# Kernel optimization log

Hardware: AMD Instinct MI355X
Metric: run time of the kernel (lower is better)

Reference implementation:

```python
import jax, jax.numpy as jnp
import numpy as np

V, D, H, L, F, S, HI, DI, TOPK = 50257, 1024, 16, 8, 4096, 1024, 4, 64, 512
DH = D // H
EPS = 1e-6


def rmsnorm(x, w):
    # matches torch: norm = ||x||_2 * D^-0.5 ; out = w * x / (norm + eps)
    n = jnp.linalg.norm(x, axis=-1, keepdims=True) * (x.shape[-1] ** -0.5)
    return w * (x / (n + EPS))


def setup_inputs() -> dict:
    key = jax.random.key(0)
    ks = jax.random.split(key, 16)
    std = 0.02
    tokens = jax.random.randint(ks[0], (2, S), 0, V)
    embed_w = jax.random.normal(ks[1], (V, D), jnp.float32) * std
    pos_w = jax.random.normal(ks[2], (S, D), jnp.float32) * std
    wq = jax.random.normal(ks[3], (L, D, D), jnp.float32) * std
    wk = jax.random.normal(ks[4], (L, D, D), jnp.float32) * std
    wv = jax.random.normal(ks[5], (L, D, D), jnp.float32) * std
    wo = jax.random.normal(ks[6], (L, D, D), jnp.float32) * std
    iq = jax.random.normal(ks[7], (L, D, HI * DI), jnp.float32) * std
    ik = jax.random.normal(ks[8], (L, D, DI), jnp.float32) * std
    iw = jax.random.normal(ks[9], (L, D, HI), jnp.float32) * std
    w1 = jax.random.normal(ks[10], (L, D, F), jnp.float32) * std
    w2 = jax.random.normal(ks[11], (L, F, D), jnp.float32) * std
    norm1 = jnp.ones((L, D), jnp.float32)
    norm2 = jnp.ones((L, D), jnp.float32)
    norm_f = jnp.ones((D,), jnp.float32)
    return dict(tokens=tokens, embed_w=embed_w, pos_w=pos_w, wq=wq, wk=wk,
                wv=wv, wo=wo, iq=iq, ik=ik, iw=iw, w1=w1, w2=w2,
                norm1=norm1, norm2=norm2, norm_f=norm_f)


def _block(x, p, causal):
    (wq, wk, wv, wo, iq, ik, iw, w1, w2, n1, n2) = p
    B = x.shape[0]
    NEG = jnp.finfo(x.dtype).min
    h = rmsnorm(x, n1)
    # --- lightning indexer: scores [B, S, S] ---
    qi = (h @ iq).reshape(B, S, HI, DI)          # [B,S,HI,DI]
    ki = h @ ik                                   # [B,S,DI]
    wt = h @ iw                                   # [B,S,HI]
    idx_logits = jax.nn.relu(jnp.einsum('bqhd,bkd->bhqk', qi, ki))
    idx_scores = jnp.einsum('bqh,bhqk->bqk', wt, idx_logits)  # [B,S,S]
    masked_idx = jnp.where(causal, idx_scores, NEG)
    _, top_i = jax.lax.top_k(masked_idx, TOPK)    # [B,S,TOPK]
    bi = jnp.arange(B)[:, None, None]
    qix = jnp.arange(S)[None, :, None]
    topk_mask = jnp.zeros((B, S, S), bool).at[bi, qix, top_i].set(True)
    allowed = causal & topk_mask                  # [B,S,S]
    # --- sparse multi-head attention (masked dense form, same math) ---
    q = (h @ wq).reshape(B, S, H, DH)
    k = (h @ wk).reshape(B, S, H, DH)
    v = (h @ wv).reshape(B, S, H, DH)
    att = jnp.einsum('bqhd,bkhd->bhqk', q, k) / jnp.sqrt(jnp.float32(DH))
    att = jnp.where(allowed[:, None, :, :], att, NEG)
    p_att = jax.nn.softmax(att, axis=-1)
    out = jnp.einsum('bhqk,bkhd->bqhd', p_att, v).reshape(B, S, D) @ wo
    x = x + out
    # --- feed-forward (exact GELU as nn.GELU) ---
    h2 = rmsnorm(x, n2)
    x = x + jax.nn.gelu(h2 @ w1, approximate=False) @ w2
    return x


def reference(tokens, embed_w, pos_w, wq, wk, wv, wo, iq, ik, iw, w1, w2,
              norm1, norm2, norm_f):
    x = embed_w[tokens] + pos_w[None, :tokens.shape[1], :]
    causal = jnp.tril(jnp.ones((S, S), bool))[None]  # [1,S,S]

    def step(x, p):
        return _block(x, p, causal), None

    x, _ = jax.lax.scan(step, x, (wq, wk, wv, wo, iq, ik, iw, w1, w2, norm1, norm2))
    x = rmsnorm(x, norm_f)
    logits = x @ embed_w.T  # tied lm_head
    return logits
```

## Files before the change

kernel.cpp:

```cpp
#include <hip/hip_runtime.h>
#include <cstdint>
#include <cstddef>

#define S_LEN 1024
#define D_DIM 1024
#define NH 16
#define DHD 64
#define NL 8
#define FF_DIM 4096
#define HI_N 4
#define DI_N 64
#define TOPK_N 512
#define BSROWS 2048
#define VOCAB 50257
#define VPAD 50304
#define NTILES_V 393
#define YPX 50

#define QKV_LD 3072
#define IDX_LD 384
#define COL_QI 0
#define COL_KI 256
#define COL_WT 320

#define NEGF -3.0e38f

typedef __attribute__((ext_vector_type(8))) _Float16 half8;
typedef __attribute__((ext_vector_type(4))) _Float16 half4v;
typedef __attribute__((ext_vector_type(4))) float f32x4;

#if __has_builtin(__builtin_amdgcn_mfma_f32_16x16x16f16)
#define MFMA16F(a, b, c) __builtin_amdgcn_mfma_f32_16x16x16f16((a), (b), (c), 0, 0, 0)
#else
static __device__ __forceinline__ f32x4 mfma16f_asm(half4v a, half4v b, f32x4 c) {
  f32x4 d;
  asm volatile("v_mfma_f32_16x16x16_f16 %0, %1, %2, %3\n\ts_nop 7\n\ts_nop 7"
               : "=v"(d) : "v"(a), "v"(b), "v"(c));
  return d;
}
#define MFMA16F(a, b, c) mfma16f_asm((a), (b), (c))
#endif

typedef const __attribute__((address_space(1))) void* gas_ptr;
typedef __attribute__((address_space(3))) void* las_ptr;
__device__ __forceinline__ void gload16(const void* g, void* l) {
#if __has_builtin(__builtin_amdgcn_global_load_lds)
  __builtin_amdgcn_global_load_lds((gas_ptr)g, (las_ptr)l, 16, 0, 0);
#else
  *(uint4*)l = *(const uint4*)g;
#endif
}

__device__ __forceinline__ short f2h(float x) {
  _Float16 h = (_Float16)x;
  return *reinterpret_cast<short*>(&h);
}
__device__ __forceinline__ float h2f(short b) {
  _Float16 h = *reinterpret_cast<_Float16*>(&b);
  return (float)h;
}
__device__ __forceinline__ void split_h(float x, short& hi, short& lo) {
  hi = f2h(x);
  lo = f2h(x - h2f(hi));
}

__global__ __launch_bounds__(256) void embed_kernel(
    const int* __restrict__ tokens, const float* __restrict__ E,
    const float* __restrict__ P, float* __restrict__ X)
{
  int bs = blockIdx.x;
  int s = bs & (S_LEN - 1);
  int tid = threadIdx.x;
  int tok = tokens[bs];
  float4 e = ((const float4*)(E + (size_t)tok * D_DIM))[tid];
  float4 p = ((const float4*)(P + (size_t)s * D_DIM))[tid];
  float4 o; o.x = e.x + p.x; o.y = e.y + p.y; o.z = e.z + p.z; o.w = e.w + p.w;
  ((float4*)(X + (size_t)bs * D_DIM))[tid] = o;
}

__global__ __launch_bounds__(256) void cvt_embed_kernel(
    const float* __restrict__ E, short* __restrict__ Eh)
{
  const long valid4 = (long)VOCAB * D_DIM / 4;
  const long total4 = (long)VPAD * D_DIM / 4;
  long i = (long)blockIdx.x * 256 + threadIdx.x;
  long stride = (long)gridDim.x * 256;
  for (; i < total4; i += stride) {
    short4 o = make_short4(0, 0, 0, 0);
    if (i < valid4) {
      float4 v = ((const float4*)E)[i];
      o = make_short4(f2h(v.x), f2h(v.y), f2h(v.z), f2h(v.w));
    }
    ((short4*)Eh)[i] = o;
  }
}

__global__ __launch_bounds__(256) void rmsnorm_split_kernel(
    const float* __restrict__ X, const float* __restrict__ W,
    short* __restrict__ O )
{
  int r = blockIdx.x;
  int tid = threadIdx.x;
  float4 v = ((const float4*)(X + (size_t)r * D_DIM))[tid];
  float ss = v.x * v.x + v.y * v.y + v.z * v.z + v.w * v.w;
  __shared__ float red[4];
  __shared__ float sh_inv;
  for (int o = 32; o; o >>= 1) ss += __shfl_down(ss, o);
  if ((tid & 63) == 0) red[tid >> 6] = ss;
  __syncthreads();
  if (tid == 0) {
    float s = red[0] + red[1] + red[2] + red[3];
    sh_inv = 1.0f / (sqrtf(s) * 0.03125f + 1e-6f);
  }
  __syncthreads();
  float inv = sh_inv;
  float4 w = ((const float4*)W)[tid];
  float o0 = w.x * v.x * inv, o1 = w.y * v.y * inv;
  float o2 = w.z * v.z * inv, o3 = w.w * v.w * inv;
  short4 hi, lo;
  split_h(o0, hi.x, lo.x); split_h(o1, hi.y, lo.y);
  split_h(o2, hi.z, lo.z); split_h(o3, hi.w, lo.w);
  ((short4*)(O + (size_t)r * D_DIM))[tid] = hi;
  ((short4*)(O + (size_t)BSROWS * D_DIM + (size_t)r * D_DIM))[tid] = lo;
}

__global__ __launch_bounds__(256) void rmsnorm_h_kernel(
    const float* __restrict__ X, const float* __restrict__ W, short* __restrict__ O)
{
  int r = blockIdx.x;
  int tid = threadIdx.x;
  float4 v = ((const float4*)(X + (size_t)r * D_DIM))[tid];
  float ss = v.x * v.x + v.y * v.y + v.z * v.z + v.w * v.w;
  __shared__ float red[4];
  __shared__ float sh_inv;
  for (int o = 32; o; o >>= 1) ss += __shfl_down(ss, o);
  if ((tid & 63) == 0) red[tid >> 6] = ss;
  __syncthreads();
  if (tid == 0) {
    float s = red[0] + red[1] + red[2] + red[3];
    sh_inv = 1.0f / (sqrtf(s) * 0.03125f + 1e-6f);
  }
  __syncthreads();
  float inv = sh_inv;
  float4 w = ((const float4*)W)[tid];
  short4 o4 = make_short4(f2h(w.x * v.x * inv), f2h(w.y * v.y * inv),
                          f2h(w.z * v.z * inv), f2h(w.w * v.w * inv));
  ((short4*)(O + (size_t)r * D_DIM))[tid] = o4;
}

__global__ __launch_bounds__(256) void packT_all_kernel(
    const float* __restrict__ W0, short* __restrict__ BT0, int K, int N)
{
  __shared__ float t[32][33];
  int z = blockIdx.z;
  const float* W = W0 + (size_t)z * K * N;
  short* BT = BT0 + (size_t)z * N * K;
  int n0 = blockIdx.x * 32, k0 = blockIdx.y * 32;
  int tx = threadIdx.x, ty = threadIdx.y;
#pragma unroll
  for (int r = 0; r < 32; r += 8)
    t[ty + r][tx] = W[(size_t)(k0 + ty + r) * N + n0 + tx];
  __syncthreads();
#pragma unroll
  for (int r = 0; r < 32; r += 8)
    BT[(size_t)(n0 + ty + r) * K + k0 + tx] = f2h(t[tx][ty + r]);
}

__global__ __launch_bounds__(256) void pack_qkv_all_kernel(
    const float* __restrict__ wq0, const float* __restrict__ wk0,
    const float* __restrict__ wv0, short* __restrict__ BT0)
{
  __shared__ float t[32][33];
  int z = blockIdx.z;
  const float* wq = wq0 + (size_t)z * D_DIM * D_DIM;
  const float* wk = wk0 + (size_t)z * D_DIM * D_DIM;
  const float* wv = wv0 + (size_t)z * D_DIM * D_DIM;
  short* BT = BT0 + (size_t)z * QKV_LD * D_DIM;
  int n0 = blockIdx.x * 32, k0 = blockIdx.y * 32;
  int tx = threadIdx.x, ty = threadIdx.y;
  const float* src = (n0 < 1024) ? wq : (n0 < 2048) ? wk : wv;
  int c0 = n0 & 1023;
#pragma unroll
  for (int r = 0; r < 32; r += 8)
    t[ty + r][tx] = src[(size_t)(k0 + ty + r) * 1024 + c0 + tx];
  __syncthreads();
#pragma unroll
  for (int r = 0; r < 32; r += 8)
    BT[(size_t)(n0 + ty + r) * D_DIM + k0 + tx] = f2h(t[tx][ty + r]);
}

__global__ __launch_bounds__(256) void pack_idx_all_kernel(
    const float* __restrict__ iq0, const float* __restrict__ ik0,
    const float* __restrict__ iw0, short* __restrict__ BT0)
{
  __shared__ float t[32][33];
  const size_t plane = (size_t)IDX_LD * D_DIM;
  int z = blockIdx.z;
  const float* iq = iq0 + (size_t)z * D_DIM * (HI_N * DI_N);
  const float* ik = ik0 + (size_t)z * D_DIM * DI_N;
  const float* iw = iw0 + (size_t)z * D_DIM * HI_N;
  short* BT = BT0 + (size_t)z * 2 * plane;
  int n0 = blockIdx.x * 32, k0 = blockIdx.y * 32;
  int tx = threadIdx.x, ty = threadIdx.y;
  const float* src = nullptr; int ld = 0, c0 = 0;
  if (n0 < 256)      { src = iq; ld = 256; c0 = n0; }
  else if (n0 < 320) { src = ik; ld = 64;  c0 = n0 - 256; }
  else if (n0 < 352) { src = iw; ld = 4;   c0 = n0 - 320; }
#pragma unroll
  for (int r = 0; r < 32; r += 8) {
    float v = 0.f;
    int c = c0 + tx;
    if (src && c < ld) v = src[(size_t)(k0 + ty + r) * ld + c];
    t[ty + r][tx] = v;
  }
  __syncthreads();
#pragma unroll
  for (int r = 0; r < 32; r += 8) {
    short hi, lo;
    split_h(t[tx][ty + r], hi, lo);
    size_t o = (size_t)(n0 + ty + r) * D_DIM + k0 + tx;
    BT[o] = hi;
    BT[plane + o] = lo;
  }
}

#define RA 40

template<int BM>
__global__ __launch_bounds__(256) void gemm_split_kernel(
    const short* __restrict__ A, size_t aplane,
    const short* __restrict__ BT, size_t bplane,
    float* __restrict__ C, int M, int N, int K)
{
  constexpr int MI = BM / 32;
  __shared__ short Al[2 * BM * RA];
  __shared__ short Bl[2 * 128 * RA];
  int tid = threadIdx.x;
  int wave = tid >> 6, lane = tid & 63;
  int wr = (wave >> 1) * (BM / 2), wc = (wave & 1) * 64;
  int lr = lane & 15, lk = lane >> 4;
  int m0 = blockIdx.y * BM, n0 = blockIdx.x * 128;
  f32x4 acc[MI][4] = {};

  for (int k0 = 0; k0 < K; k0 += 32) {
    __syncthreads();
#pragma unroll
    for (int f = 0; f < BM / 32; ++f) {
      int idx = tid + f * 256;
      int p = idx / (BM * 4), r2 = idx % (BM * 4);
      int row = r2 >> 2, sub = r2 & 3;
      uint4 v = *(const uint4*)(A + (size_t)p * aplane + (size_t)(m0 + row) * K + k0 + sub * 8);
      *(uint4*)(Al + p * BM * RA + row * RA + sub * 8) = v;
    }
#pragma unroll
    for (int f = 0; f < 4; ++f) {
      int idx = tid + f * 256;
      int p = idx >> 9, r2 = idx & 511;
      int row = r2 >> 2, sub = r2 & 3;
      uint4 v = *(const uint4*)(BT + (size_t)p * bplane + (size_t)(n0 + row) * K + k0 + sub * 8);
      *(uint4*)(Bl + p * 128 * RA + row * RA + sub * 8) = v;
    }
    __syncthreads();
    half8 ah[MI], al_[MI], bh[4], bl_[4];
#pragma unroll
    for (int i = 0; i < MI; ++i) {
      ah[i] = *(const half8*)(Al + (wr + i * 16 + lr) * RA + lk * 8);
      al_[i] = *(const half8*)(Al + BM * RA + (wr + i * 16 + lr) * RA + lk * 8);
    }
#pragma unroll
    for (int j = 0; j < 4; ++j) {
      bh[j] = *(const half8*)(Bl + (wc + j * 16 + lr) * RA + lk * 8);
      bl_[j] = *(const half8*)(Bl + 128 * RA + (wc + j * 16 + lr) * RA + lk * 8);
    }
#pragma unroll
    for (int i = 0; i < MI; ++i)
#pragma unroll
      for (int j = 0; j < 4; ++j) {
        f32x4 a = acc[i][j];
        a = __builtin_amdgcn_mfma_f32_16x16x32_f16(al_[i], bh[j], a, 0, 0, 0);
        a = __builtin_amdgcn_mfma_f32_16x16x32_f16(ah[i], bl_[j], a, 0, 0, 0);
        a = __builtin_amdgcn_mfma_f32_16x16x32_f16(ah[i], bh[j], a, 0, 0, 0);
        acc[i][j] = a;
      }
  }
#pragma unroll
  for (int i = 0; i < MI; ++i)
#pragma unroll
    for (int r = 0; r < 4; ++r) {
      int m = m0 + wr + i * 16 + lk * 4 + r;
#pragma unroll
      for (int j = 0; j < 4; ++j) {
        int n = n0 + wc + j * 16 + lr;
        if (n < N) C[(size_t)m * N + n] = acc[i][j][r];
      }
    }
}

template<int BM, int EPI>
__global__ __launch_bounds__(256) void gemm_g_kernel(
    const short* __restrict__ A, const short* __restrict__ BT,
    const float* __restrict__ R, void* __restrict__ C, int M, int N, int K)
{
  constexpr int MI = BM / 32;
  constexpr int AF = (BM >= 64) ? BM / 64 : 1;
  __shared__ short Al[2][BM * 32];
  __shared__ short Bl[2][128 * 32];
  int tid = threadIdx.x;
  int wave = tid >> 6, lane = tid & 63;
  int wr = (wave >> 1) * (BM / 2), wc = (wave & 1) * 64;
  int lr = lane & 15, lk = lane >> 4;
  int m0 = blockIdx.y * BM, n0 = blockIdx.x * 128;
  f32x4 acc[MI][4] = {};

  const short* ap[AF]; int ad[AF];
#pragma unroll
  for (int f = 0; f < AF; ++f) {
    int idx = tid + f * 256;
    int row = idx >> 2, slot = idx & 3;
    ap[f] = A + (size_t)(m0 + row) * K + ((slot ^ (row & 3)) * 8);
    ad[f] = idx * 8;
  }
  const bool a_act = (BM >= 64) || (tid < BM * 4);
  const short* bp[2]; int bd[2];
#pragma unroll
  for (int f = 0; f < 2; ++f) {
    int idx = tid + f * 256;
    int row = idx >> 2, slot = idx & 3;
    bp[f] = BT + (size_t)(n0 + row) * K + ((slot ^ (row & 3)) * 8);
    bd[f] = idx * 8;
  }
  int aoff[MI], boff[4];
#pragma unroll
  for (int i = 0; i < MI; ++i) {
    int row = wr + i * 16 + lr;
    aoff[i] = row * 32 + ((lk ^ (row & 3)) * 8);
  }
#pragma unroll
  for (int j = 0; j < 4; ++j) {
    int row = wc + j * 16 + lr;
    boff[j] = row * 32 + ((lk ^ (row & 3)) * 8);
  }

#pragma unroll
  for (int f = 0; f < AF; ++f)
    if (a_act) { gload16(ap[f], &Al[0][ad[f]]); ap[f] += 32; }
#pragma unroll
  for (int f = 0; f < 2; ++f) { gload16(bp[f], &Bl[0][bd[f]]); bp[f] += 32; }
  __syncthreads();

  const int nt = K >> 5;
  int cur = 0;
  for (int t = 0; t < nt; ++t) {
    if (t + 1 < nt) {
#pragma unroll
      for (int f = 0; f < AF; ++f)
        if (a_act) { gload16(ap[f], &Al[cur ^ 1][ad[f]]); ap[f] += 32; }
#pragma unroll
      for (int f = 0; f < 2; ++f) { gload16(bp[f], &Bl[cur ^ 1][bd[f]]); bp[f] += 32; }
    }
    half8 af[MI], bfr[4];
#pragma unroll
    for (int i = 0; i < MI; ++i) af[i] = *(const half8*)(&Al[cur][aoff[i]]);
#pragma unroll
    for (int j = 0; j < 4; ++j) bfr[j] = *(const half8*)(&Bl[cur][boff[j]]);
#pragma unroll
    for (int i = 0; i < MI; ++i)
#pragma unroll
      for (int j = 0; j < 4; ++j)
        acc[i][j] = __builtin_amdgcn_mfma_f32_16x16x32_f16(af[i], bfr[j], acc[i][j], 0, 0, 0);
    __syncthreads();
    cur ^= 1;
  }
#pragma unroll
  for (int i = 0; i < MI; ++i)
#pragma unroll
    for (int r = 0; r < 4; ++r) {
      int m = m0 + wr + i * 16 + lk * 4 + r;
#pragma unroll
      for (int j = 0; j < 4; ++j) {
        int n = n0 + wc + j * 16 + lr;
        float v = acc[i][j][r];
        if (EPI == 1) {
          ((short*)C)[(size_t)m * N + n] = f2h(v);
        } else if (EPI == 2) {
          v = 0.5f * v * (1.0f + erff(v * 0.70710678118654752f));
          ((short*)C)[(size_t)m * N + n] = f2h(v);
        } else {
          ((float*)C)[(size_t)m * N + n] = v + R[(size_t)m * N + n];
        }
      }
    }
}

__global__ __launch_bounds__(256) void gemm_logits_g_kernel(
    const short* __restrict__ A, const short* __restrict__ BT,
    float* __restrict__ C, int M, int N, int K)
{
  int bid = blockIdx.x;
  int xcd = bid & 7, idx0 = bid >> 3;
  int mt = idx0 & 15, yt = (idx0 >> 4) + xcd * YPX;
  if (yt >= NTILES_V) return;
  int m0 = mt * 128, n0 = yt * 128;

  __shared__ short Al[2][128 * 32];
  __shared__ short Bl[2][128 * 32];
  int tid = threadIdx.x;
  int wave = tid >> 6, lane = tid & 63;
  int wr = (wave >> 1) * 64, wc = (wave & 1) * 64;
  int lr = lane & 15, lk = lane >> 4;
  f32x4 acc[4][4] = {};

  const short* ap[2]; int ad[2];
  const short* bp[2]; int bd[2];
#pragma unroll
  for (int f = 0; f < 2; ++f) {
    int idx = tid + f * 256;
    int row = idx >> 2, slot = idx & 3;
    ap[f] = A + (size_t)(m0 + row) * K + ((slot ^ (row & 3)) * 8);
    ad[f] = idx * 8;
    bp[f] = BT + (size_t)(n0 + row) * K + ((slot ^ (row & 3)) * 8);
    bd[f] = idx * 8;
  }
  int aoff[4], boff[4];
#pragma unroll
  for (int i = 0; i < 4; ++i) {
    int row = wr + i * 16 + lr;
    aoff[i] = row * 32 + ((lk ^ (row & 3)) * 8);
    int rowb = wc + i * 16 + lr;
    boff[i] = rowb * 32 + ((lk ^ (rowb & 3)) * 8);
  }

#pragma unroll
  for (int f = 0; f < 2; ++f) { gload16(ap[f], &Al[0][ad[f]]); ap[f] += 32; }
#pragma unroll
  for (int f = 0; f < 2; ++f) { gload16(bp[f], &Bl[0][bd[f]]); bp[f] += 32; }
  __syncthreads();

  const int nt = K >> 5;
  int cur = 0;
  for (int t = 0; t < nt; ++t) {
    if (t + 1 < nt) {
#pragma unroll
      for (int f = 0; f < 2; ++f) { gload16(ap[f], &Al[cur ^ 1][ad[f]]); ap[f] += 32; }
#pragma unroll
      for (int f = 0; f < 2; ++f) { gload16(bp[f], &Bl[cur ^ 1][bd[f]]); bp[f] += 32; }
    }
    half8 af[4], bfr[4];
#pragma unroll
    for (int i = 0; i < 4; ++i) af[i] = *(const half8*)(&Al[cur][aoff[i]]);
#pragma unroll
    for (int j = 0; j < 4; ++j) bfr[j] = *(const half8*)(&Bl[cur][boff[j]]);
#pragma unroll
    for (int i = 0; i < 4; ++i)
#pragma unroll
      for (int j = 0; j < 4; ++j)
        acc[i][j] = __builtin_amdgcn_mfma_f32_16x16x32_f16(af[i], bfr[j], acc[i][j], 0, 0, 0);
    __syncthreads();
    cur ^= 1;
  }
#pragma unroll
  for (int i = 0; i < 4; ++i)
#pragma unroll
    for (int r = 0; r < 4; ++r) {
      int m = m0 + wr + i * 16 + lk * 4 + r;
#pragma unroll
      for (int j = 0; j < 4; ++j) {
        int n = n0 + wc + j * 16 + lr;
        if (n < N) C[(size_t)m * N + n] = acc[i][j][r];
      }
    }
}

__global__ __launch_bounds__(256) void gemm_logits_f32b_kernel(
    const short* __restrict__ A, const float* __restrict__ BT,
    float* __restrict__ C, int M, int N, int K)
{
  __shared__ short Al[128 * RA];
  __shared__ short Bl[128 * RA];
  int tid = threadIdx.x;
  int wave = tid >> 6, lane = tid & 63;
  int wr = (wave >> 1) * 64, wc = (wave & 1) * 64;
  int lr = lane & 15, lk = lane >> 4;
  int m0 = blockIdx.y * 128, n0 = blockIdx.x * 128;
  f32x4 acc[4][4] = {};

  for (int k0 = 0; k0 < K; k0 += 32) {
    __syncthreads();
#pragma unroll
    for (int f = 0; f < 2; ++f) {
      int idx = tid + f * 256, row = idx >> 2, sub = idx & 3;
      uint4 v = *(const uint4*)(A + (size_t)(m0 + row) * K + k0 + sub * 8);
      *(uint4*)(Al + row * RA + sub * 8) = v;
    }
#pragma unroll
    for (int f = 0; f < 4; ++f) {
      int idx = tid + f * 256, row = idx >> 3, qq = idx & 7;
      int gn = n0 + row;
      float4 v = make_float4(0.f, 0.f, 0.f, 0.f);
      if (gn < N) v = *(const float4*)(BT + (size_t)gn * K + k0 + qq * 4);
      *(short4*)(Bl + row * RA + qq * 4) =
          make_short4(f2h(v.x), f2h(v.y), f2h(v.z), f2h(v.w));
    }
    __syncthreads();
    half8 af[4], bfr[4];
#pragma unroll
    for (int i = 0; i < 4; ++i)
      af[i] = *(const half8*)(Al + (wr + i * 16 + lr) * RA + lk * 8);
#pragma unroll
    for (int j = 0; j < 4; ++j)
      bfr[j] = *(const half8*)(Bl + (wc + j * 16 + lr) * RA + lk * 8);
#pragma unroll
    for (int i = 0; i < 4; ++i)
#pragma unroll
      for (int j = 0; j < 4; ++j)
        acc[i][j] = __builtin_amdgcn_mfma_f32_16x16x32_f16(af[i], bfr[j], acc[i][j], 0, 0, 0);
  }
#pragma unroll
  for (int i = 0; i < 4; ++i)
#pragma unroll
    for (int r = 0; r < 4; ++r) {
      int m = m0 + wr + i * 16 + lk * 4 + r;
#pragma unroll
      for (int j = 0; j < 4; ++j) {
        int n = n0 + wc + j * 16 + lr;
        if (n < N) C[(size_t)m * N + n] = acc[i][j][r];
      }
    }
}

__device__ __forceinline__ unsigned int ford(float f) {
  unsigned int u = __float_as_uint(f);
  return (u & 0x80000000u) ? ~u : (u | 0x80000000u);
}

__global__ __launch_bounds__(256) void idx_topk_kernel(
    const float* __restrict__ Hx, unsigned int* __restrict__ MASK)
{
  int bq = blockIdx.x;
  int q = bq & (S_LEN - 1);
  int b = bq >> 10;
  int tid = threadIdx.x;
  int n = q + 1;
  if (n <= TOPK_N) {
    if (tid < 32) {
      int full = n >> 5, rem = n & 31;
      unsigned int w = 0u;
      if (tid < full) w = 0xFFFFFFFFu;
      else if (tid == full && rem) w = (1u << rem) - 1u;
      MASK[(size_t)bq * 32 + tid] = w;
    }
    return;
  }
  __shared__ float qi_s[HI_N * DI_N];
  __shared__ float wt_s[HI_N];
  __shared__ float sc[S_LEN];
  __shared__ unsigned long long keys[S_LEN];
  __shared__ unsigned int mw[32];
  qi_s[tid] = Hx[(size_t)bq * IDX_LD + COL_QI + tid];
  if (tid < HI_N) wt_s[tid] = Hx[(size_t)bq * IDX_LD + COL_WT + tid];
  __syncthreads();
  for (int k = tid; k < n; k += 256) {
    const float* kr = Hx + (size_t)(b * S_LEN + k) * IDX_LD + COL_KI;
    float d0 = 0.f, d1 = 0.f, d2 = 0.f, d3 = 0.f;
#pragma unroll
    for (int d = 0; d < DI_N; ++d) {
      float kv = kr[d];
      d0 = fmaf(qi_s[d], kv, d0);
      d1 = fmaf(qi_s[64 + d], kv, d1);
      d2 = fmaf(qi_s[128 + d], kv, d2);
      d3 = fmaf(qi_s[192 + d], kv, d3);
    }
    sc[k] = wt_s[0] * fmaxf(d0, 0.f) + wt_s[1] * fmaxf(d1, 0.f)
          + wt_s[2] * fmaxf(d2, 0.f) + wt_s[3] * fmaxf(d3, 0.f);
  }
  __syncthreads();
  for (int i = tid; i < S_LEN; i += 256) {
    unsigned long long kk = 0ull;
    if (i < n) kk = ((unsigned long long)ford(sc[i]) << 32) | (unsigned int)(S_LEN - 1 - i);
    keys[i] = kk;
  }
  __syncthreads();
  for (int size = 2; size <= S_LEN; size <<= 1) {
    for (int stride = size >> 1; stride > 0; stride >>= 1) {
      for (int t = tid; t < S_LEN / 2; t += 256) {
        int j = t & (stride - 1);
        int lo = ((t ^ j) << 1) | j;
        int hi = lo | stride;
        unsigned long long a = keys[lo], c = keys[hi];
        bool desc = ((lo & size) == 0);
        bool sw = desc ? (a < c) : (a > c);
        if (sw) { keys[lo] = c; keys[hi] = a; }
      }
      __syncthreads();
    }
  }
  if (tid < 32) mw[tid] = 0u;
  __syncthreads();
  for (int i = tid; i < TOPK_N; i += 256) {
    int k = S_LEN - 1 - (int)(keys[i] & 0xFFFFFFFFull);
    atomicOr(&mw[k >> 5], 1u << (k & 31));
  }
  __syncthreads();
  if (tid < 32) MASK[(size_t)bq * 32 + tid] = mw[tid];
}

__global__ __launch_bounds__(256) void attn_mfma_kernel(
    const short* __restrict__ QKV, const unsigned int* __restrict__ MASK,
    short* __restrict__ O )
{
  __shared__ short Kl[2][64 * 64];
  __shared__ short Vtl[2][64 * 68];
  int i = blockIdx.x;
  int p = i >> 5;
  int qt = (p < 8) ? p : 23 - p;
  int h = (i >> 1) & 15;
  int b = i & 1;
  int tid = threadIdx.x;
  int w = tid >> 6, l = tid & 63;
  int lq = l & 15, g = l >> 4;
  int q0 = qt * 64;
  const short* Kb = QKV + (size_t)b * S_LEN * QKV_LD + 1024 + h * DHD;
  const short* Vb = QKV + (size_t)b * S_LEN * QKV_LD + 2048 + h * DHD;
  int vu = tid >> 1, vhalf = tid & 1, vkg = vu >> 3, vdg = vu & 7;
  const int mrow = w * 16 + lq;
  const unsigned int* mp = MASK + (size_t)(b * S_LEN + q0 + mrow) * 32;

  half8 qf[2];
  {
    const short* qrow = QKV + ((size_t)(b * S_LEN + q0 + mrow)) * QKV_LD + h * DHD;
    qf[0] = *(const half8*)(qrow + g * 8);
    qf[1] = *(const half8*)(qrow + 32 + g * 8);
  }
  unsigned int mw0 = mp[0], mw1 = mp[1];
  {
#pragma unroll
    for (int i2 = 0; i2 < 2; ++i2) {
      int idx = tid + i2 * 256;
      int row = idx >> 3, sub = idx & 7;
      gload16(Kb + (size_t)row * QKV_LD + (size_t)((sub ^ (row & 7)) * 8), &Kl[0][idx * 8]);
    }
    int krow = vkg * 4 + vhalf * 2;
    uint4 v0 = *(const uint4*)(Vb + (size_t)krow * QKV_LD + vdg * 8);
    uint4 v1 = *(const uint4*)(Vb + (size_t)(krow + 1) * QKV_LD + vdg * 8);
    const short* s0 = (const short*)&v0;
    const short* s1 = (const short*)&v1;
#pragma unroll
    for (int j = 0; j < 8; ++j)
      *(short2*)(&Vtl[0][(vdg * 8 + j) * 68 + vkg * 4 + vhalf * 2]) = make_short2(s0[j], s1[j]);
  }
  __syncthreads();

  f32x4 acc_o[4] = {};
  float m_run = -1.0e30f, l_run = 0.f;
  int cur = 0;

  for (int kt = 0; kt <= qt; ++kt) {
    bool more = kt < qt;
    uint4 v0, v1;
    unsigned int nmw0 = 0u, nmw1 = 0u;
    if (more) {
#pragma unroll
      for (int i2 = 0; i2 < 2; ++i2) {
        int idx = tid + i2 * 256;
        int row = idx >> 3, sub = idx & 7;
        gload16(Kb + (size_t)((kt + 1) * 64 + row) * QKV_LD + (size_t)((sub ^ (row & 7)) * 8),
                &Kl[cur ^ 1][idx * 8]);
      }
      int krow = (kt + 1) * 64 + vkg * 4 + vhalf * 2;
      v0 = *(const uint4*)(Vb + (size_t)krow * QKV_LD + vdg * 8);
      v1 = *(const uint4*)(Vb + (size_t)(krow + 1) * QKV_LD + vdg * 8);
      nmw0 = mp[2 * (kt + 1)];
      nmw1 = mp[2 * (kt + 1) + 1];
    }
    f32x4 s[4] = {};
    __builtin_amdgcn_s_setprio(1);
#pragma unroll
    for (int ks = 0; ks < 4; ++ks) {
      half8 kf0 = *(const half8*)(&Kl[cur][(ks * 16 + lq) * 64 + ((g ^ (lq & 7)) * 8)]);
      half8 kf1 = *(const half8*)(&Kl[cur][(ks * 16 + lq) * 64 + (((4 + g) ^ (lq & 7)) * 8)]);
      s[ks] = __builtin_amdgcn_mfma_f32_16x16x32_f16(kf0, qf[0], s[ks], 0, 0, 0);
      s[ks] = __builtin_amdgcn_mfma_f32_16x16x32_f16(kf1, qf[1], s[ks], 0, 0, 0);
    }
    __builtin_amdgcn_s_setprio(0);
    float mx = NEGF;
#pragma unroll
    for (int ks = 0; ks < 4; ++ks) {
      unsigned int mwv = (ks < 2) ? mw0 : mw1;
      int bb = (ks & 1) * 16 + g * 4;
#pragma unroll
      for (int r = 0; r < 4; ++r) {
        float sv = ((mwv >> (bb + r)) & 1u) ? s[ks][r] * 0.125f : NEGF;
        s[ks][r] = sv;
        mx = fmaxf(mx, sv);
      }
    }
    mx = fmaxf(mx, __shfl_xor(mx, 16));
    mx = fmaxf(mx, __shfl_xor(mx, 32));
    float m_new = fmaxf(m_run, mx);
    float scale = __expf(m_run - m_new);
    float lsum = 0.f;
    half4v pf[4];
#pragma unroll
    for (int ks = 0; ks < 4; ++ks) {
      half4v t;
#pragma unroll
      for (int r = 0; r < 4; ++r) {
        float pp = __expf(s[ks][r] - m_new);
        lsum += pp;
        t[r] = (_Float16)pp;
      }
      pf[ks] = t;
    }
    lsum += __shfl_xor(lsum, 16);
    lsum += __shfl_xor(lsum, 32);
    l_run = l_run * scale + lsum;
    m_run = m_new;
    float sc[4];
#pragma unroll
    for (int r = 0; r < 4; ++r) sc[r] = __shfl(scale, g * 4 + r);
    __builtin_amdgcn_s_setprio(1);
#pragma unroll
    for (int dt = 0; dt < 4; ++dt) {
      f32x4 a = acc_o[dt];
      a[0] *= sc[0]; a[1] *= sc[1]; a[2] *= sc[2]; a[3] *= sc[3];
#pragma unroll
      for (int ks = 0; ks < 4; ++ks) {
        half4v vf = *(const half4v*)(&Vtl[cur][(dt * 16 + lq) * 68 + ks * 16 + g * 4]);
        a = MFMA16F(pf[ks], vf, a);
      }
      acc_o[dt] = a;
    }
    __builtin_amdgcn_s_setprio(0);
    if (more) {
      const short* s0 = (const short*)&v0;
      const short* s1 = (const short*)&v1;
#pragma unroll
      for (int j = 0; j < 8; ++j)
        *(short2*)(&Vtl[cur ^ 1][(vdg * 8 + j) * 68 + vkg * 4 + vhalf * 2]) = make_short2(s0[j], s1[j]);
      mw0 = nmw0;
      mw1 = nmw1;
    }
    __syncthreads();
    cur ^= 1;
  }
  float linv[4];
#pragma unroll
  for (int r = 0; r < 4; ++r) linv[r] = 1.0f / __shfl(l_run, g * 4 + r);
#pragma unroll
  for (int dt = 0; dt < 4; ++dt)
#pragma unroll
    for (int r = 0; r < 4; ++r) {
      int q = q0 + w * 16 + g * 4 + r;
      float o = acc_o[dt][r] * linv[r];
      O[(size_t)(b * S_LEN + q) * D_DIM + h * DHD + dt * 16 + lq] = f2h(o);
    }
}

extern "C" void kernel_launch(void* const* d_in, const int* in_sizes, int n_in,
                              void* d_out, int out_size, void* d_ws, size_t ws_size,
                              hipStream_t stream) {
  (void)in_sizes; (void)n_in; (void)out_size;
  const int*   tokens  = (const int*)d_in[0];
  const float* embed_w = (const float*)d_in[1];
  const float* pos_w   = (const float*)d_in[2];
  const float* wq      = (const float*)d_in[3];
  const float* wk      = (const float*)d_in[4];
  const float* wv      = (const float*)d_in[5];
  const float* wo      = (const float*)d_in[6];
  const float* iqw     = (const float*)d_in[7];
  const float* ikw     = (const float*)d_in[8];
  const float* iww     = (const float*)d_in[9];
  const float* w1      = (const float*)d_in[10];
  const float* w2      = (const float*)d_in[11];
  const float* n1      = (const float*)d_in[12];
  const float* n2      = (const float*)d_in[13];
  const float* nf      = (const float*)d_in[14];
  float* logits = (float*)d_out;

  short* Hh = (short*)d_ws;
  size_t need_eh = ((size_t)BSROWS * D_DIM + (size_t)VPAD * D_DIM) * 2;
  bool use_eh = ws_size >= need_eh;
  short* Eh = Hh + (size_t)BSROWS * D_DIM;

  char* base = (char*)d_out;
  size_t off = (size_t)BSROWS * D_DIM * 4;
  float* X = logits;
  float* Hx = (float*)(base + off);    off += (size_t)BSROWS * IDX_LD * 4;
  short* QKVh = (short*)(base + off);  off += (size_t)BSROWS * QKV_LD * 2;
  short* Hsp = (short*)(base + off);   off += (size_t)2 * BSROWS * D_DIM * 2;
  short* AOh = (short*)(base + off);   off += (size_t)BSROWS * D_DIM * 2;
  short* FFh = (short*)(base + off);   off += (size_t)BSROWS * FF_DIM * 2;
  unsigned int* MASKb = (unsigned int*)(base + off); off += (size_t)BSROWS * 32 * 4;
  short* BTqkvA = (short*)(base + off); off += (size_t)NL * QKV_LD * D_DIM * 2;
  short* BTidxA = (short*)(base + off); off += (size_t)NL * 2 * IDX_LD * D_DIM * 2;
  short* BTwoA = (short*)(base + off);  off += (size_t)NL * D_DIM * D_DIM * 2;
  short* BTw1A = (short*)(base + off);  off += (size_t)NL * FF_DIM * D_DIM * 2;
  short* BTw2A = (short*)(base + off);  off += (size_t)NL * FF_DIM * D_DIM * 2;

  const size_t plH  = (size_t)BSROWS * D_DIM;
  const size_t plIx = (size_t)IDX_LD * D_DIM;

  hipLaunchKernelGGL(embed_kernel, dim3(BSROWS), dim3(256), 0, stream,
                     tokens, embed_w, pos_w, X);
  if (use_eh)
    hipLaunchKernelGGL(cvt_embed_kernel, dim3(8192), dim3(256), 0, stream, embed_w, Eh);

  hipLaunchKernelGGL(pack_qkv_all_kernel, dim3(QKV_LD / 32, 32, NL), dim3(32, 8), 0, stream,
                     wq, wk, wv, BTqkvA);
  hipLaunchKernelGGL(pack_idx_all_kernel, dim3(IDX_LD / 32, 32, NL), dim3(32, 8), 0, stream,
                     iqw, ikw, iww, BTidxA);
  hipLaunchKernelGGL(packT_all_kernel, dim3(32, 32, NL), dim3(32, 8), 0, stream,
                     wo, BTwoA, D_DIM, D_DIM);
  hipLaunchKernelGGL(packT_all_kernel, dim3(FF_DIM / 32, 32, NL), dim3(32, 8), 0, stream,
                     w1, BTw1A, D_DIM, FF_DIM);
  hipLaunchKernelGGL(packT_all_kernel, dim3(D_DIM / 32, FF_DIM / 32, NL), dim3(32, 8), 0, stream,
                     w2, BTw2A, FF_DIM, D_DIM);

  for (int l = 0; l < NL; ++l) {
    short* BTqkv = BTqkvA + (size_t)l * QKV_LD * D_DIM;
    short* BTidx = BTidxA + (size_t)l * 2 * IDX_LD * D_DIM;
    short* BTwo  = BTwoA + (size_t)l * D_DIM * D_DIM;
    short* BTw1  = BTw1A + (size_t)l * FF_DIM * D_DIM;
    short* BTw2  = BTw2A + (size_t)l * FF_DIM * D_DIM;

    hipLaunchKernelGGL(rmsnorm_split_kernel, dim3(BSROWS), dim3(256), 0, stream,
                       X, n1 + (size_t)l * D_DIM, Hsp);
    hipLaunchKernelGGL((gemm_g_kernel<64, 1>), dim3(QKV_LD / 128, 32), dim3(256), 0, stream,
                       Hsp, BTqkv, nullptr, QKVh, BSROWS, QKV_LD, D_DIM);
    hipLaunchKernelGGL((gemm_split_kernel<32>), dim3(IDX_LD / 128, 64), dim3(256), 0, stream,
                       Hsp, plH, BTidx, plIx, Hx, BSROWS, IDX_LD, D_DIM);
    hipLaunchKernelGGL(idx_topk_kernel, dim3(BSROWS), dim3(256), 0, stream, Hx, MASKb);
    hipLaunchKernelGGL(attn_mfma_kernel, dim3(512), dim3(256), 0, stream,
                       QKVh, MASKb, AOh);
    hipLaunchKernelGGL((gemm_g_kernel<32, 3>), dim3(8, 64), dim3(256), 0, stream,
                       AOh, BTwo, X, X, BSROWS, D_DIM, D_DIM);
    hipLaunchKernelGGL(rmsnorm_h_kernel, dim3(BSROWS), dim3(256), 0, stream,
                       X, n2 + (size_t)l * D_DIM, Hsp);
    hipLaunchKernelGGL((gemm_g_kernel<64, 2>), dim3(FF_DIM / 128, 32), dim3(256), 0, stream,
                       Hsp, BTw1, nullptr, FFh, BSROWS, FF_DIM, D_DIM);
    hipLaunchKernelGGL((gemm_g_kernel<32, 3>), dim3(8, 64), dim3(256), 0, stream,
                       FFh, BTw2, X, X, BSROWS, D_DIM, FF_DIM);
  }

  hipLaunchKernelGGL(rmsnorm_h_kernel, dim3(BSROWS), dim3(256), 0, stream, X, nf, Hh);
  if (use_eh) {
    hipLaunchKernelGGL(gemm_logits_g_kernel, dim3(8 * YPX * 16), dim3(256), 0, stream,
                       Hh, Eh, logits, BSROWS, VOCAB, D_DIM);
  } else {
    hipLaunchKernelGGL(gemm_logits_f32b_kernel, dim3((VOCAB + 127) / 128, 16), dim3(256), 0, stream,
                       Hh, embed_w, logits, BSROWS, VOCAB, D_DIM);
  }
}
```

Before: 3.299 ms.

## Use 256x256 tiles with 4-stage pipelined loads in logits GEMM

Rewrites the tied lm_head logits GEMM to use 256x256 output tiles computed by 512-thread blocks, with each wave computing a 128x64 sub-tile. It replaces double buffering with a 4-deep LDS ring: three tiles are prefetched ahead, explicit vmcnt waits and raw barriers stand in for __syncthreads, and s_setprio is raised around the MFMA burst. The vocabulary padding grows to a multiple of 256. The goal is more operand reuse per loaded byte and better hiding of global-load latency, at the cost of 128KB of LDS per block, one block per CU, and higher register pressure.

```diff
diff --git a/kernel.cpp b/kernel.cpp
--- a/kernel.cpp
+++ b/kernel.cpp
@@ -13,9 +13,9 @@
 #define TOPK_N 512
 #define BSROWS 2048
 #define VOCAB 50257
-#define VPAD 50304
-#define NTILES_V 393
-#define YPX 50
+#define VPAD2 50432
+#define NT256 197
+#define YPX2 25
 
 #define QKV_LD 3072
 #define IDX_LD 384
@@ -82,7 +82,7 @@
     const float* __restrict__ E, short* __restrict__ Eh)
 {
   const long valid4 = (long)VOCAB * D_DIM / 4;
-  const long total4 = (long)VPAD * D_DIM / 4;
+  const long total4 = (long)VPAD2 * D_DIM / 4;
   long i = (long)blockIdx.x * 256 + threadIdx.x;
   long stride = (long)gridDim.x * 256;
   for (; i < total4; i += stride) {
@@ -392,83 +392,101 @@
     }
 }
 
-__global__ __launch_bounds__(256) void gemm_logits_g_kernel(
+__global__ __launch_bounds__(512, 1) void gemm_logits_p_kernel(
     const short* __restrict__ A, const short* __restrict__ BT,
     float* __restrict__ C, int M, int N, int K)
 {
   int bid = blockIdx.x;
   int xcd = bid & 7, idx0 = bid >> 3;
-  int mt = idx0 & 15, yt = (idx0 >> 4) + xcd * YPX;
-  if (yt >= NTILES_V) return;
-  int m0 = mt * 128, n0 = yt * 128;
-
-  __shared__ short Al[2][128 * 32];
-  __shared__ short Bl[2][128 * 32];
+  int mt = idx0 & 7, yt = (idx0 >> 3) + xcd * YPX2;
+  if (yt >= NT256) return;
+  int m0 = mt * 256, n0 = yt * 256;
+
+  __shared__ short As[4][256 * 32];
+  __shared__ short Bs[4][256 * 32];
   int tid = threadIdx.x;
   int wave = tid >> 6, lane = tid & 63;
-  int wr = (wave >> 1) * 64, wc = (wave & 1) * 64;
+  int wm = wave >> 2, wn = wave & 3;
   int lr = lane & 15, lk = lane >> 4;
-  f32x4 acc[4][4] = {};
-
-  const short* ap[2]; int ad[2];
-  const short* bp[2]; int bd[2];
+  f32x4 acc[8][4] = {};
+
+  const short* apg[2]; int adl[2];
+  const short* bpg[2]; int bdl[2];
 #pragma unroll
   for (int f = 0; f < 2; ++f) {
-    int idx = tid + f * 256;
+    int idx = tid + f * 512;
     int row = idx >> 2, slot = idx & 3;
-    ap[f] = A + (size_t)(m0 + row) * K + ((slot ^ (row & 3)) * 8);
-    ad[f] = idx * 8;
-    bp[f] = BT + (size_t)(n0 + row) * K + ((slot ^ (row & 3)) * 8);
-    bd[f] = idx * 8;
-  }
-  int aoff[4], boff[4];
-#pragma unroll
-  for (int i = 0; i < 4; ++i) {
-    int row = wr + i * 16 + lr;
+    apg[f] = A + (size_t)(m0 + row) * K + ((slot ^ (row & 3)) * 8);
+    bpg[f] = BT + (size_t)(n0 + row) * K + ((slot ^ (row & 3)) * 8);
+    adl[f] = idx * 8;
+    bdl[f] = idx * 8;
+  }
+  int aoff[8], boff[4];
+#pragma unroll
+  for (int i = 0; i < 8; ++i) {
+    int row = wm * 128 + i * 16 + lr;
     aoff[i] = row * 32 + ((lk ^ (row & 3)) * 8);
-    int rowb = wc + i * 16 + lr;
-    boff[i] = rowb * 32 + ((lk ^ (rowb & 3)) * 8);
-  }
-
-#pragma unroll
-  for (int f = 0; f < 2; ++f) { gload16(ap[f], &Al[0][ad[f]]); ap[f] += 32; }
-#pragma unroll
-  for (int f = 0; f < 2; ++f) { gload16(bp[f], &Bl[0][bd[f]]); bp[f] += 32; }
-  __syncthreads();
+  }
+#pragma unroll
+  for (int j = 0; j < 4; ++j) {
+    int row = wn * 64 + j * 16 + lr;
+    boff[j] = row * 32 + ((lk ^ (row & 3)) * 8);
+  }
+
+#define STAGE_TILE(buf)                                              \
+  {                                                                  \
+    _Pragma("unroll")                                                \
+    for (int f = 0; f < 2; ++f) {                                    \
+      gload16(apg[f], &As[buf][adl[f]]); apg[f] += 32;               \
+      gload16(bpg[f], &Bs[buf][bdl[f]]); bpg[f] += 32;               \
+    }                                                                \
+  }
 
   const int nt = K >> 5;
-  int cur = 0;
+  STAGE_TILE(0);
+  STAGE_TILE(1);
+  STAGE_TILE(2);
+  asm volatile("s_waitcnt vmcnt(8)" ::: "memory");
+  __builtin_amdgcn_s_barrier();
+
   for (int t = 0; t < nt; ++t) {
-    if (t + 1 < nt) {
-#pragma unroll
-      for (int f = 0; f < 2; ++f) { gload16(ap[f], &Al[cur ^ 1][ad[f]]); ap[f] += 32; }
-#pragma unroll
-      for (int f = 0; f < 2; ++f) { gload16(bp[f], &Bl[cur ^ 1][bd[f]]); bp[f] += 32; }
-    }
-    half8 af[4], bfr[4];
-#pragma unroll
-    for (int i = 0; i < 4; ++i) af[i] = *(const half8*)(&Al[cur][aoff[i]]);
-#pragma unroll
-    for (int j = 0; j < 4; ++j) bfr[j] = *(const half8*)(&Bl[cur][boff[j]]);
-#pragma unroll
-    for (int i = 0; i < 4; ++i)
+    int cur = t & 3;
+    half8 af[8], bfr[4];
+#pragma unroll
+    for (int i = 0; i < 8; ++i) af[i] = *(const half8*)(&As[cur][aoff[i]]);
+#pragma unroll
+    for (int j = 0; j < 4; ++j) bfr[j] = *(const half8*)(&Bs[cur][boff[j]]);
+    __builtin_amdgcn_s_setprio(1);
+#pragma unroll
+    for (int i = 0; i < 8; ++i)
 #pragma unroll
       for (int j = 0; j < 4; ++j)
         acc[i][j] = __builtin_amdgcn_mfma_f32_16x16x32_f16(af[i], bfr[j], acc[i][j], 0, 0, 0);
-    __syncthreads();
-    cur ^= 1;
-  }
-#pragma unroll
-  for (int i = 0; i < 4; ++i)
+    __builtin_amdgcn_s_setprio(0);
+    __builtin_amdgcn_s_barrier();
+    if (t + 3 < nt) {
+      STAGE_TILE((t + 3) & 3);
+      asm volatile("s_waitcnt vmcnt(8)" ::: "memory");
+    } else if (t + 2 < nt) {
+      asm volatile("s_waitcnt vmcnt(4)" ::: "memory");
+    } else if (t + 1 < nt) {
+      asm volatile("s_waitcnt vmcnt(0)" ::: "memory");
+    }
+    __builtin_amdgcn_s_barrier();
+  }
+
+#pragma unroll
+  for (int i = 0; i < 8; ++i)
 #pragma unroll
     for (int r = 0; r < 4; ++r) {
-      int m = m0 + wr + i * 16 + lk * 4 + r;
+      int m = m0 + wm * 128 + i * 16 + lk * 4 + r;
 #pragma unroll
       for (int j = 0; j < 4; ++j) {
-        int n = n0 + wc + j * 16 + lr;
+        int n = n0 + wn * 64 + j * 16 + lr;
         if (n < N) C[(size_t)m * N + n] = acc[i][j][r];
       }
     }
+#undef STAGE_TILE
 }
 
 __global__ __launch_bounds__(256) void gemm_logits_f32b_kernel(
@@ -778,7 +796,7 @@
   float* logits = (float*)d_out;
 
   short* Hh = (short*)d_ws;
-  size_t need_eh = ((size_t)BSROWS * D_DIM + (size_t)VPAD * D_DIM) * 2;
+  size_t need_eh = ((size_t)BSROWS * D_DIM + (size_t)VPAD2 * D_DIM) * 2;
   bool use_eh = ws_size >= need_eh;
   short* Eh = Hh + (size_t)BSROWS * D_DIM;
 
@@ -844,7 +862,7 @@
 
   hipLaunchKernelGGL(rmsnorm_h_kernel, dim3(BSROWS), dim3(256), 0, stream, X, nf, Hh);
   if (use_eh) {
-    hipLaunchKernelGGL(gemm_logits_g_kernel, dim3(8 * YPX * 16), dim3(256), 0, stream,
+    hipLaunchKernelGGL(gemm_logits_p_kernel, dim3(8 * YPX2 * 8), dim3(512), 0, stream,
                        Hh, Eh, logits, BSROWS, VOCAB, D_DIM);
   } else {
     hipLaunchKernelGGL(gemm_logits_f32b_kernel, dim3((VOCAB + 127) / 128, 16), dim3(256), 0, stream,
```

Measured after the change: 3.389 ms. 2.7% more time.
